# Kernel tuning notes

Measured on AMD Instinct MI355X. Metric: run time of the kernel, lower is better.

Reference implementation:

```python
import jax, jax.numpy as jnp
import numpy as np

B, T, I, H, L, C = 64, 512, 512, 1024, 4, 1000


def _gru_layer(x_seq, Wih, Whh, bih, bhh):
    """Run one GRU layer over the full sequence.
    x_seq: [B, T, In]; Wih: [3H, In]; Whh: [3H, H]; bih, bhh: [3H].
    Returns (outputs [B, T, H], final hidden [B, H]).
    GRUCell math (PyTorch):
      r = sigmoid(Wir x + bir + Whr h + bhr)
      z = sigmoid(Wiz x + biz + Whz h + bhz)
      n = tanh(Win x + bin + r * (Whn h + bhn))
      h' = (1 - z) * n + z * h
    """
    # Precompute all input-side gate projections in one big GEMM: [B,T,3H]
    gx = jnp.einsum('bti,gi->btg', x_seq, Wih) + bih
    gx = jnp.moveaxis(gx, 1, 0)  # [T, B, 3H] for scan
    h0 = jnp.zeros((x_seq.shape[0], Whh.shape[1]), dtype=x_seq.dtype)

    def step(h, gx_t):
        gh = h @ Whh.T + bhh                       # [B, 3H]
        xr, xz, xn = jnp.split(gx_t, 3, axis=-1)
        hr, hz, hn = jnp.split(gh, 3, axis=-1)
        r = jax.nn.sigmoid(xr + hr)
        z = jax.nn.sigmoid(xz + hz)
        n = jnp.tanh(xn + r * hn)
        h_new = (1.0 - z) * n + z * h
        return h_new, h_new

    h_last, ys = jax.lax.scan(step, h0, gx)
    return jnp.moveaxis(ys, 0, 1), h_last


def setup_inputs() -> dict:
    key = jax.random.key(0)
    ks = jax.random.split(key, 2 + 4 * L + 2)
    inp = {"x": jax.random.normal(ks[0], (B, T, I), dtype=jnp.float32)}
    s = 1.0 / np.sqrt(H)  # PyTorch GRUCell init scale
    kidx = 1
    for l in range(L):
        in_dim = I if l == 0 else H
        inp[f"Wih{l}"] = jax.random.uniform(ks[kidx + 0], (3 * H, in_dim), minval=-s, maxval=s, dtype=jnp.float32)
        inp[f"Whh{l}"] = jax.random.uniform(ks[kidx + 1], (3 * H, H), minval=-s, maxval=s, dtype=jnp.float32)
        inp[f"bih{l}"] = jax.random.uniform(ks[kidx + 2], (3 * H,), minval=-s, maxval=s, dtype=jnp.float32)
        inp[f"bhh{l}"] = jax.random.uniform(ks[kidx + 3], (3 * H,), minval=-s, maxval=s, dtype=jnp.float32)
        kidx += 4
    inp["fc_w"] = jax.random.uniform(ks[kidx], (C, H), minval=-s, maxval=s, dtype=jnp.float32)
    inp["fc_b"] = jax.random.uniform(ks[kidx + 1], (C,), minval=-s, maxval=s, dtype=jnp.float32)
    return inp


def reference(x, Wih0, Whh0, bih0, bhh0, Wih1, Whh1, bih1, bhh1,
              Wih2, Whh2, bih2, bhh2, Wih3, Whh3, bih3, bhh3, fc_w, fc_b):
    layers = [(Wih0, Whh0, bih0, bhh0), (Wih1, Whh1, bih1, bhh1),
              (Wih2, Whh2, bih2, bhh2), (Wih3, Whh3, bih3, bhh3)]
    seq = x
    h_last = None
    for Wih, Whh, bih, bhh in layers:
        seq, h_last = _gru_layer(seq, Wih, Whh, bih, bhh)
    return h_last @ fc_w.T + fc_b  # [B, num_classes]
```

## Files before the change

### kernel.cpp

```cpp
#include <hip/hip_runtime.h>

#define B_ 64
#define T_ 512
#define IN0_ 512
#define H_ 1024
#define C_ 1000
#define NWG 256
#define NTHR 256

typedef _Float16 f16;
typedef _Float16 f16x8 __attribute__((ext_vector_type(8)));
typedef _Float16 f16x4 __attribute__((ext_vector_type(4)));
typedef float f32x4 __attribute__((ext_vector_type(4)));

struct Args {
  const float* x;
  const float* Wih[4];
  const float* Whh[4];
  const float* bih[4];
  const float* bhh[4];
  const float* fcw;
  const float* fcb;
  float* out;
  f16* wpack;
  f16* x16;
  f16* hist;
  float* h32f;
  int* flags;
  int* bar;
  int RM;
};

__device__ __forceinline__ float sigmoid_f(float x) {
  return 1.0f / (1.0f + __expf(-x));
}
__device__ __forceinline__ float tanh_f(float x) {
  return 1.0f - 2.0f / (__expf(2.0f * x) + 1.0f);
}

__device__ __forceinline__ void heavy_barrier(int* bar) {
  __threadfence();
  __syncthreads();
  if (threadIdx.x == 0) {
    int* cnt = bar;
    int* gen = bar + 1;
    int g = __hip_atomic_load(gen, __ATOMIC_RELAXED, __HIP_MEMORY_SCOPE_AGENT);
    int v = __hip_atomic_fetch_add(cnt, 1, __ATOMIC_ACQ_REL, __HIP_MEMORY_SCOPE_AGENT);
    if (v == NWG - 1) {
      __hip_atomic_store(cnt, 0, __ATOMIC_RELAXED, __HIP_MEMORY_SCOPE_AGENT);
      __hip_atomic_store(gen, g + 1, __ATOMIC_RELEASE, __HIP_MEMORY_SCOPE_AGENT);
    } else {
      int cur;
      do {
        __builtin_amdgcn_s_sleep(2);
        cur = __hip_atomic_load(gen, __ATOMIC_ACQUIRE, __HIP_MEMORY_SCOPE_AGENT);
      } while (cur == g);
    }
  }
  __syncthreads();
  __threadfence();
}

__device__ __forceinline__ void astore8(f16* p, unsigned long long v) {
  __hip_atomic_store((unsigned long long*)p, v, __ATOMIC_RELAXED,
                     __HIP_MEMORY_SCOPE_AGENT);
}
union UF32 { float f; unsigned u; };
__device__ __forceinline__ void astore4(float* p, float v) {
  UF32 c; c.f = v;
  __hip_atomic_store((unsigned*)p, c.u, __ATOMIC_RELAXED,
                     __HIP_MEMORY_SCOPE_AGENT);
}

__device__ __forceinline__ int fload(const int* f) {
  return __hip_atomic_load(f, __ATOMIC_RELAXED, __HIP_MEMORY_SCOPE_AGENT);
}

__constant__ __device__ const size_t WOFF_[4] = {0ul, 4718592ul, 11010048ul, 17301504ul};

__device__ __forceinline__ int ridx(int bank, int rb, int i, int lane) {
  return ((bank * 4 + rb) * 4 + i) * 64 + lane;
}

template <int IN, bool XA>
__device__ void run_layer(const Args& a, int layer, int sub, bool is_last,
                          float* red, float* hlds, f16* hstage) {
  constexpr int NKB = (IN + H_) / 32;
  constexpr int NXB = IN / 32;
  constexpr int SLICE = NKB / 4;

  const int tid = threadIdx.x;
  const int wave = tid >> 6;
  const int lane = tid & 63;
  const int jc = lane & 15;
  const int kg = lane >> 4;
  const int j = sub * 16 + jc;
  const int wbase = wave * SLICE;
  const int fid = layer * 64 + sub;
  const int RM = a.RM;

  const float bir = a.bih[layer][j], bhr = a.bhh[layer][j];
  const float biz = a.bih[layer][H_ + j], bhz = a.bhh[layer][H_ + j];
  const float bin_ = a.bih[layer][2 * H_ + j], bhn = a.bhh[layer][2 * H_ + j];

  const f16x8* wpb = (const f16x8*)(a.wpack + WOFF_[layer] +
                                    (size_t)sub * 3 * NKB * 512) + lane;
  f16x8 wfR[SLICE], wfZ[SLICE], wfN[SLICE];
#pragma unroll
  for (int kk = 0; kk < SLICE; ++kk) {
    wfR[kk] = wpb[(size_t)(0 * NKB + wbase + kk) * 64];
    wfZ[kk] = wpb[(size_t)(1 * NKB + wbase + kk) * 64];
    wfN[kk] = wpb[(size_t)(2 * NKB + wbase + kk) * 64];
  }

  f16* hring = a.hist + (size_t)layer * RM * B_ * H_;
  const f16* xring = XA ? a.hist + (size_t)(layer - 1) * RM * B_ * H_
                        : (const f16*)nullptr;

  for (int t = 0; t < T_; ++t) {
    {
      const int tt = tid;
      if (tt < 64) {
        if (t >= 1) {
          const int* f = a.flags + (layer * 64 + tt) * 32;
          while (fload(f) < t) __builtin_amdgcn_s_sleep(1);
        }
      } else if (tt < 128) {
        if (XA) {
          const int* f = a.flags + ((layer - 1) * 64 + (tt - 64)) * 32;
          while (fload(f) < t + 1) __builtin_amdgcn_s_sleep(1);
        }
      } else if (tt < 192) {
        if (layer < 3 && t + 1 >= RM) {
          const int* f = a.flags + ((layer + 1) * 64 + (tt - 128)) * 32;
          while (fload(f) < t + 2 - RM) __builtin_amdgcn_s_sleep(1);
        }
      }
      __syncthreads();
    }

    const f16* xbase = XA ? (xring + (size_t)((t + 1) % RM) * B_ * H_)
                          : (a.x16 + (size_t)t * B_ * IN0_);
    const f16* hbase = hring + (size_t)(t % RM) * B_ * H_;
    f16* ho = hring + (size_t)((t + 1) % RM) * B_ * H_;

    f32x4 aR[4], aZ[4], aNX[4], aNH[4];
#pragma unroll
    for (int rb = 0; rb < 4; ++rb) {
      aR[rb] = 0.f; aZ[rb] = 0.f; aNX[rb] = 0.f; aNH[rb] = 0.f;
    }

#define LOADRB(BUF, RB)                                                      \
  do {                                                                       \
    const int arow_ = (RB) * 16 + jc;                                        \
    const f16* xrow_ = xbase + (size_t)arow_ * IN + kg * 8;                  \
    const f16* hrow_ = hbase + (size_t)arow_ * H_ + kg * 8;                  \
    _Pragma("unroll")                                                        \
    for (int kk = 0; kk < SLICE; ++kk) {                                     \
      const int kb_ = wbase + kk;                                            \
      BUF[kk] = (kb_ < NXB) ? *(const f16x8*)(xrow_ + kb_ * 32)              \
                            : *(const f16x8*)(hrow_ + (kb_ - NXB) * 32);     \
    }                                                                        \
  } while (0)

#define MFMARB(BUF, RB)                                                      \
  do {                                                                       \
    _Pragma("unroll")                                                        \
    for (int kk = 0; kk < SLICE; ++kk) {                                     \
      const int kb_ = wbase + kk;                                            \
      const bool isx_ = kb_ < NXB;                                           \
      const f16x8 af_ = BUF[kk];                                             \
      aR[RB] = __builtin_amdgcn_mfma_f32_16x16x32_f16(af_, wfR[kk], aR[RB], 0, 0, 0); \
      aZ[RB] = __builtin_amdgcn_mfma_f32_16x16x32_f16(af_, wfZ[kk], aZ[RB], 0, 0, 0); \
      const f16x8 z8_ = {0, 0, 0, 0, 0, 0, 0, 0};                            \
      const f16x8 afx_ = isx_ ? af_ : z8_;                                   \
      const f16x8 afh_ = isx_ ? z8_ : af_;                                   \
      aNX[RB] = __builtin_amdgcn_mfma_f32_16x16x32_f16(afx_, wfN[kk], aNX[RB], 0, 0, 0); \
      aNH[RB] = __builtin_amdgcn_mfma_f32_16x16x32_f16(afh_, wfN[kk], aNH[RB], 0, 0, 0); \
    }                                                                        \
  } while (0)

    {
      f16x8 bufA[SLICE], bufB[SLICE];
      LOADRB(bufA, 0);
      LOADRB(bufB, 1);
      MFMARB(bufA, 0);
      LOADRB(bufA, 2);
      MFMARB(bufB, 1);
      LOADRB(bufB, 3);
      MFMARB(bufA, 2);
      MFMARB(bufB, 3);
    }
#undef LOADRB
#undef MFMARB

    if (wave < 2) {
#pragma unroll
      for (int rb = 0; rb < 4; ++rb)
#pragma unroll
        for (int i = 0; i < 4; ++i) {
          red[ridx(0 + wave, rb, i, lane)] = aR[rb][i];
          red[ridx(2 + wave, rb, i, lane)] = aZ[rb][i];
          red[ridx(4 + wave, rb, i, lane)] = aNX[rb][i];
          red[ridx(6 + wave, rb, i, lane)] = aNH[rb][i];
        }
    }
    __syncthreads();
    if (wave >= 2) {
      const int p = wave - 2;
#pragma unroll
      for (int rb = 0; rb < 4; ++rb)
#pragma unroll
        for (int i = 0; i < 4; ++i) {
          red[ridx(0 + p, rb, i, lane)] += aR[rb][i];
          red[ridx(2 + p, rb, i, lane)] += aZ[rb][i];
          red[ridx(4 + p, rb, i, lane)] += aNX[rb][i];
          red[ridx(6 + p, rb, i, lane)] += aNH[rb][i];
        }
    }
    __syncthreads();

    {
#pragma unroll
      for (int i = 0; i < 4; ++i) {
        const int b = wave * 16 + kg * 4 + i;
        const float R  = red[ridx(0, wave, i, lane)] + red[ridx(1, wave, i, lane)];
        const float Z  = red[ridx(2, wave, i, lane)] + red[ridx(3, wave, i, lane)];
        const float NX = red[ridx(4, wave, i, lane)] + red[ridx(5, wave, i, lane)];
        const float NH = red[ridx(6, wave, i, lane)] + red[ridx(7, wave, i, lane)];
        const float r = sigmoid_f(R + bir + bhr);
        const float zz = sigmoid_f(Z + biz + bhz);
        const float nn = tanh_f(NX + bin_ + r * (NH + bhn));
        const float hp = hlds[b * 17 + jc];
        const float hnew = (1.0f - zz) * nn + zz * hp;
        hlds[b * 17 + jc] = hnew;
        hstage[b * 20 + jc] = (f16)hnew;
        if (is_last && t == T_ - 1) astore4(&a.h32f[(size_t)b * H_ + j], hnew);
      }
    }
    __syncthreads();
    {
      const int b = tid >> 2;
      const int c = tid & 3;
      const unsigned long long v =
          *(const unsigned long long*)&hstage[b * 20 + c * 4];
      astore8(&ho[(size_t)b * H_ + sub * 16 + c * 4], v);
    }

    asm volatile("s_waitcnt vmcnt(0) lgkmcnt(0)" ::: "memory");
    __syncthreads();
    if (tid == 0)
      __hip_atomic_store(a.flags + fid * 32, t + 1, __ATOMIC_RELAXED,
                         __HIP_MEMORY_SCOPE_AGENT);
  }
}

__global__ void __launch_bounds__(NTHR, 1) gru_pipeline(Args a) {
  __shared__ float red[8 * 4 * 4 * 64];
  __shared__ float hlds[B_ * 17];
  __shared__ f16 hstage[B_ * 20];

  const int tid = threadIdx.x;
  const int gtid = blockIdx.x * NTHR + tid;
  const int NT = NWG * NTHR;

  {
    const int nf4 = B_ * T_ * IN0_ / 4;
    for (int i = gtid; i < nf4; i += NT) {
      int k4 = i & 127;
      int q = i >> 7;
      int b = q & 63;
      int t = q >> 6;
      const float4 v = *(const float4*)(a.x + ((size_t)b * T_ + t) * IN0_ + k4 * 4);
      f16x4 o;
      o[0] = (f16)v.x; o[1] = (f16)v.y; o[2] = (f16)v.z; o[3] = (f16)v.w;
      *(f16x4*)(a.x16 + (size_t)i * 4) = o;
    }
  }
  {
    f16x8 z8 = {0, 0, 0, 0, 0, 0, 0, 0};
    for (int i = gtid; i < 4 * B_ * H_ / 8; i += NT) {
      int l = i / (B_ * H_ / 8);
      int o = i - l * (B_ * H_ / 8);
      ((f16x8*)(a.hist + (size_t)l * a.RM * B_ * H_))[o] = z8;
    }
  }
  for (int i = tid; i < B_ * 17; i += NTHR) hlds[i] = 0.f;
  for (int l = 0; l < 4; ++l) {
    const int In = l ? H_ : IN0_;
    const int K = In + H_;
    const int NKB = K / 32;
    const float* Wih = a.Wih[l];
    const float* Whh = a.Whh[l];
    f16* wp = a.wpack + WOFF_[l];
    const int nunits = 3 * H_ * K / 8;
    for (int uu = gtid; uu < nunits; uu += NT) {
      int lane = uu & 63;
      int q = uu >> 6;
      int kb = q % NKB; q /= NKB;
      int gate = q % 3;
      int subb = q / 3;
      int j = subb * 16 + (lane & 15);
      int g = gate * H_ + j;
      int k = kb * 32 + (lane >> 4) * 8;
      const float* src = (k < In) ? (Wih + (size_t)g * In + k)
                                  : (Whh + (size_t)g * H_ + (k - In));
      f16x8 vv;
#pragma unroll
      for (int e = 0; e < 8; ++e) vv[e] = (f16)src[e];
      ((f16x8*)wp)[uu] = vv;
    }
  }

  heavy_barrier(a.bar);

  const int wg = blockIdx.x;
  const int xslot = wg & 7;
  const int layer = xslot >> 1;
  const int sub = (wg >> 3) * 2 + (xslot & 1);

  if (layer == 0) run_layer<IN0_, false>(a, layer, sub, false, red, hlds, hstage);
  else            run_layer<H_, true>(a, layer, sub, layer == 3, red, hlds, hstage);

  heavy_barrier(a.bar);

  for (int o = gtid; o < B_ * C_; o += NT) {
    const int b = o / C_;
    const int c = o - b * C_;
    const float* hv = a.h32f + (size_t)b * H_;
    const float* wv = a.fcw + (size_t)c * H_;
    float s = a.fcb[c];
    for (int k = 0; k < H_; k += 4) {
      const float4 h4 = *(const float4*)(hv + k);
      const float4 w4 = *(const float4*)(wv + k);
      s = fmaf(h4.x, w4.x, s);
      s = fmaf(h4.y, w4.y, s);
      s = fmaf(h4.z, w4.z, s);
      s = fmaf(h4.w, w4.w, s);
    }
    a.out[o] = s;
  }
}

extern "C" void kernel_launch(void* const* d_in, const int* in_sizes, int n_in,
                              void* d_out, int out_size, void* d_ws, size_t ws_size,
                              hipStream_t stream) {
  Args a;
  a.x = (const float*)d_in[0];
  for (int l = 0; l < 4; ++l) {
    a.Wih[l] = (const float*)d_in[1 + 4 * l];
    a.Whh[l] = (const float*)d_in[2 + 4 * l];
    a.bih[l] = (const float*)d_in[3 + 4 * l];
    a.bhh[l] = (const float*)d_in[4 + 4 * l];
  }
  a.fcw = (const float*)d_in[17];
  a.fcb = (const float*)d_in[18];
  a.out = (float*)d_out;

  const size_t fixed = 23592960ul * 2
                     + 16777216ul * 2
                     + (size_t)B_ * H_ * 4
                     + NWG * 32 * sizeof(int) + 256;
  const int cand[] = {T_ + 1, 257, 129, 65, 33, 17};
  int RM = 17;
  for (int i = 0; i < 6; ++i) {
    size_t need = fixed + 4ul * cand[i] * B_ * H_ * 2;
    if (need <= ws_size) { RM = cand[i]; break; }
  }
  a.RM = RM;

  char* ws = (char*)d_ws;
  size_t off = 0;
  a.wpack = (f16*)(ws + off); off += 23592960ul * 2;
  a.x16   = (f16*)(ws + off); off += 16777216ul * 2;
  a.hist  = (f16*)(ws + off); off += 4ul * RM * B_ * H_ * 2;
  a.h32f  = (float*)(ws + off); off += (size_t)B_ * H_ * 4;
  a.flags = (int*)(ws + off); off += NWG * 32 * sizeof(int);
  a.bar   = (int*)(ws + off); off += 256;

  hipMemsetAsync(a.flags, 0, NWG * 32 * sizeof(int) + 256, stream);

  void* params[] = { &a };
  hipError_t err = hipLaunchCooperativeKernel((void*)gru_pipeline, dim3(NWG),
                                              dim3(NTHR), params, 0, stream);
  if (err != hipSuccess) {
    gru_pipeline<<<dim3(NWG), dim3(NTHR), 0, stream>>>(a);
  }
}
```

Measured before the change: 7.984 ms.

## Aggregate per-layer step flags into a single clock and split wave waits

```diff
diff --git a/kernel.cpp b/kernel.cpp
--- a/kernel.cpp
+++ b/kernel.cpp
@@ -27,6 +27,7 @@
   f16* hist;
   float* h32f;
   int* flags;
+  int* clk;
   int* bar;
   int RM;
 };
@@ -75,6 +76,9 @@
 __device__ __forceinline__ int fload(const int* f) {
   return __hip_atomic_load(f, __ATOMIC_RELAXED, __HIP_MEMORY_SCOPE_AGENT);
 }
+__device__ __forceinline__ void fstore(int* f, int v) {
+  __hip_atomic_store(f, v, __ATOMIC_RELAXED, __HIP_MEMORY_SCOPE_AGENT);
+}
 
 __constant__ __device__ const size_t WOFF_[4] = {0ul, 4718592ul, 11010048ul, 17301504ul};
 
@@ -88,6 +92,7 @@
   constexpr int NKB = (IN + H_) / 32;
   constexpr int NXB = IN / 32;
   constexpr int SLICE = NKB / 4;
+  constexpr int HSTART = (IN == IN0_) ? 1 : 2;
 
   const int tid = threadIdx.x;
   const int wave = tid >> 6;
@@ -118,25 +123,36 @@
                         : (const f16*)nullptr;
 
   for (int t = 0; t < T_; ++t) {
-    {
-      const int tt = tid;
-      if (tt < 64) {
+    if (sub == 0) {
+      if (wave >= HSTART) {
         if (t >= 1) {
-          const int* f = a.flags + (layer * 64 + tt) * 32;
+          const int* f = a.flags + (layer * 64 + lane) * 32;
           while (fload(f) < t) __builtin_amdgcn_s_sleep(1);
         }
-      } else if (tt < 128) {
-        if (XA) {
-          const int* f = a.flags + ((layer - 1) * 64 + (tt - 64)) * 32;
-          while (fload(f) < t + 1) __builtin_amdgcn_s_sleep(1);
-        }
-      } else if (tt < 192) {
-        if (layer < 3 && t + 1 >= RM) {
-          const int* f = a.flags + ((layer + 1) * 64 + (tt - 128)) * 32;
-          while (fload(f) < t + 2 - RM) __builtin_amdgcn_s_sleep(1);
+        if (wave == HSTART && lane == 0)
+          fstore(a.clk + layer * 32, t);
+      } else if (XA) {
+        if (lane == 0) {
+          const int* c = a.clk + (layer - 1) * 32;
+          while (fload(c) < t + 1) __builtin_amdgcn_s_sleep(1);
         }
       }
-      __syncthreads();
+    } else {
+      if (wave >= HSTART) {
+        if (t >= 1 && lane == 0) {
+          const int* c = a.clk + layer * 32;
+          while (fload(c) < t) __builtin_amdgcn_s_sleep(1);
+        }
+      } else if (XA) {
+        if (lane == 0) {
+          const int* c = a.clk + (layer - 1) * 32;
+          while (fload(c) < t + 1) __builtin_amdgcn_s_sleep(1);
+        }
+      }
+    }
+    if (wave == 3 && lane == 1 && layer < 3 && t + 1 >= RM) {
+      const int* c = a.clk + (layer + 1) * 32;
+      while (fload(c) < t + 2 - RM) __builtin_amdgcn_s_sleep(1);
     }
 
     const f16* xbase = XA ? (xring + (size_t)((t + 1) % RM) * B_ * H_)
@@ -249,9 +265,13 @@
 
     asm volatile("s_waitcnt vmcnt(0) lgkmcnt(0)" ::: "memory");
     __syncthreads();
-    if (tid == 0)
-      __hip_atomic_store(a.flags + fid * 32, t + 1, __ATOMIC_RELAXED,
-                         __HIP_MEMORY_SCOPE_AGENT);
+    if (tid == 0) fstore(a.flags + fid * 32, t + 1);
+  }
+
+  if (sub == 0 && layer < 3 && wave == 0) {
+    const int* f = a.flags + (layer * 64 + lane) * 32;
+    while (fload(f) < T_) __builtin_amdgcn_s_sleep(1);
+    if (lane == 0) fstore(a.clk + layer * 32, T_);
   }
 }
 
@@ -360,7 +380,7 @@
   const size_t fixed = 23592960ul * 2
                      + 16777216ul * 2
                      + (size_t)B_ * H_ * 4
-                     + NWG * 32 * sizeof(int) + 256;
+                     + NWG * 32 * sizeof(int) + 4 * 32 * sizeof(int) + 256;
   const int cand[] = {T_ + 1, 257, 129, 65, 33, 17};
   int RM = 17;
   for (int i = 0; i < 6; ++i) {
@@ -376,9 +396,11 @@
   a.hist  = (f16*)(ws + off); off += 4ul * RM * B_ * H_ * 2;
   a.h32f  = (float*)(ws + off); off += (size_t)B_ * H_ * 4;
   a.flags = (int*)(ws + off); off += NWG * 32 * sizeof(int);
+  a.clk   = (int*)(ws + off); off += 4 * 32 * sizeof(int);
   a.bar   = (int*)(ws + off); off += 256;
 
-  hipMemsetAsync(a.flags, 0, NWG * 32 * sizeof(int) + 256, stream);
+  hipMemsetAsync(a.flags, 0,
+                 NWG * 32 * sizeof(int) + 4 * 32 * sizeof(int) + 256, stream);
 
   void* params[] = { &a };
   hipError_t err = hipLaunchCooperativeKernel((void*)gru_pipeline, dim3(NWG),
```

Result: faster. 7.777 ms (-2.6%).
